# Kernel optimization log

Hardware: AMD Instinct MI355X
Metric: run time of the kernel (lower is better)

The kernel has to match this reference:

```python
import jax, jax.numpy as jnp
import numpy as np

B = 4          # number of prefill sequences (uniform cu_seqlens)
S = 1024       # tokens per sequence; total_tokens = B*S
SCALE = 0.08838834764831845  # head_dim ** -0.5


def setup_inputs() -> dict:
    key = jax.random.key(0)
    k1, k2, k3 = jax.random.split(key, 3)
    N, H, Hk, D = B * S, 16, 4, 128
    q = jax.random.normal(k1, (N, H, D), dtype=jnp.float32)
    k = jax.random.normal(k2, (N, Hk, D), dtype=jnp.float32)
    v = jax.random.normal(k3, (N, Hk, D), dtype=jnp.float32)
    k_cache = jnp.zeros((N, Hk * D), dtype=jnp.float32)
    v_cache = jnp.zeros((N, Hk * D), dtype=jnp.float32)
    slot_mapping = jnp.arange(N, dtype=jnp.int32)
    return {"q": q, "k": k, "v": v, "k_cache": k_cache,
            "v_cache": v_cache, "slot_mapping": slot_mapping}


def _store_kvcache(k, v, k_cache, v_cache, slot_mapping):
    # scatter token KV into flat paged cache; slot == -1 means skip
    N = k.shape[0]
    valid = slot_mapping >= 0
    slot = jnp.where(valid, slot_mapping, 0)
    k_flat = k.reshape(N, -1)
    v_flat = v.reshape(N, -1)
    kc = k_cache.at[slot].set(jnp.where(valid[:, None], k_flat, k_cache[slot]))
    vc = v_cache.at[slot].set(jnp.where(valid[:, None], v_flat, v_cache[slot]))
    return kc, vc


def _varlen_causal_attn(q, k, v):
    # q: [N, H, D], k/v: [N, Hk, D] with N = B*S uniform sequences (GQA)
    N, H, D = q.shape
    Hk = k.shape[1]
    G = H // Hk
    qb = q.reshape(B, S, Hk, G, D)
    kb = k.reshape(B, S, Hk, D)
    vb = v.reshape(B, S, Hk, D)
    # scores: [B, Hk, G, Sq, Sk]
    scores = jnp.einsum("bqhgd,bkhd->bhgqk", qb, kb) * jnp.float32(SCALE)
    causal = jnp.tril(jnp.ones((S, S), dtype=bool))  # [Sq, Sk]
    scores = jnp.where(causal, scores, jnp.float32(-1e30))
    p = jax.nn.softmax(scores, axis=-1)
    o = jnp.einsum("bhgqk,bkhd->bqhgd", p, vb)
    return o.reshape(N, H, D)


def reference(q, k, v, k_cache, v_cache, slot_mapping):
    kc, vc = _store_kvcache(k, v, k_cache, v_cache, slot_mapping)
    o = _varlen_causal_attn(q, k, v)
    return o, kc, vc
```

## Files before the change

kernel.cpp:

```cpp
#include <hip/hip_runtime.h>

typedef short bf16x8 __attribute__((ext_vector_type(8)));
typedef short bf16x4 __attribute__((ext_vector_type(4)));
typedef float f32x4 __attribute__((ext_vector_type(4)));
typedef float f32x16 __attribute__((ext_vector_type(16)));

#define NB 4
#define SS 1024
#define NH 16
#define NHK 4
#define DD 128
#define NT 16
#define QSCALE 0.08838834764831845f
#define LOG2E 1.4426950408889634f

__device__ __forceinline__ float exp2v(float x) { return __builtin_amdgcn_exp2f(x); }

__device__ __forceinline__ short f2bf(float f) {
  unsigned u = __builtin_bit_cast(unsigned, f);
  u += 0x7fffu + ((u >> 16) & 1u);
  return (short)(u >> 16);
}
__device__ __forceinline__ unsigned pk2(float lo, float hi) {
  return ((unsigned)(unsigned short)f2bf(hi) << 16) | (unsigned)(unsigned short)f2bf(lo);
}

typedef __attribute__((address_space(1))) const unsigned gu32;
typedef __attribute__((address_space(3))) unsigned lu32;
__device__ __forceinline__ void gload16(const void* g, void* l) {
  __builtin_amdgcn_global_load_lds((gu32*)g, (lu32*)l, 16, 0, 0);
}

#define DRAIN_DMA()                                    \
  do {                                                 \
    asm volatile("s_waitcnt vmcnt(0)" ::: "memory");   \
    __builtin_amdgcn_sched_barrier(0);                 \
  } while (0)

__global__ __launch_bounds__(256) void scatter_kv_kernel(
    const float* __restrict__ k, const float* __restrict__ v,
    const int* __restrict__ slot, float* __restrict__ ko, float* __restrict__ vo) {
  int gid = blockIdx.x * blockDim.x + threadIdx.x;
  int tok = gid >> 7;
  int j = gid & 127;
  int s = slot[tok];
  if (s < 0) return;
  ((float4*)(ko + (size_t)s * 512))[j] = ((const float4*)(k + (size_t)tok * 512))[j];
  ((float4*)(vo + (size_t)s * 512))[j] = ((const float4*)(v + (size_t)tok * 512))[j];
}

__global__ __launch_bounds__(256) void prep_kernel(
    const float* __restrict__ k, const float* __restrict__ v,
    const int* __restrict__ slot,
    short* __restrict__ kimg, short* __restrict__ vimg,
    float* __restrict__ ko, float* __restrict__ vo) {
  __shared__ float lvf[64 * 129];
  const int blk = blockIdx.x;
  const int t = blk & 15;
  const int hk = (blk >> 4) & 3;
  const int b = blk >> 6;
  const long tb = (long)b * SS + t * 64;
  const int tid = threadIdx.x;
  short* ki = kimg + (size_t)blk * 8192;
  short* vi = vimg + (size_t)blk * 8192;

#pragma unroll
  for (int p = 0; p < 4; ++p) {
    int c = p * 256 + tid;
    int byte0 = c * 16;
    int row = byte0 >> 8;
    int d0 = (byte0 & 255) >> 1;
    const float* src = k + ((tb + row) * NHK + hk) * DD + d0;
    float4 x = *(const float4*)src;
    float4 y = *(const float4*)(src + 4);
    uint4 pk = {pk2(x.x, x.y), pk2(x.z, x.w), pk2(y.x, y.y), pk2(y.z, y.w)};
    *(uint4*)((char*)ki + (byte0 ^ ((row & 15) << 4))) = pk;
    const float* vs = v + ((tb + row) * NHK + hk) * DD + d0;
    float4 vx = *(const float4*)vs;
    float4 vy = *(const float4*)(vs + 4);
    int sl = slot[tb + row];
    if (sl >= 0) {
      float* kd = ko + (size_t)sl * 512 + hk * 128 + d0;
      *(float4*)kd = x; *(float4*)(kd + 4) = y;
      float* vd = vo + (size_t)sl * 512 + hk * 128 + d0;
      *(float4*)vd = vx; *(float4*)(vd + 4) = vy;
    }
    float* dst = &lvf[row * 129 + d0];
    dst[0] = vx.x; dst[1] = vx.y; dst[2] = vx.z; dst[3] = vx.w;
    dst[4] = vy.x; dst[5] = vy.y; dst[6] = vy.z; dst[7] = vy.w;
  }
  __syncthreads();
#pragma unroll
  for (int p = 0; p < 4; ++p) {
    int c16 = p * 256 + tid;
    int d = c16 >> 3;
    int kv0 = (c16 & 7) << 3;
    float f[8];
#pragma unroll
    for (int j = 0; j < 8; ++j) f[j] = lvf[(kv0 + j) * 129 + d];
    uint4 pk = {pk2(f[0], f[1]), pk2(f[2], f[3]), pk2(f[4], f[5]), pk2(f[6], f[7])};
    int dest = (d << 7) + ((kv0 << 1) ^ ((d & 7) << 4));
    *(uint4*)((char*)vi + dest) = pk;
  }
}

__global__ __launch_bounds__(256, 2) void attn_kernel(
    const float* __restrict__ q, const short* __restrict__ kimg,
    const short* __restrict__ vimg, float* __restrict__ o) {
  __shared__ __align__(16) short lk[2][64 * 128];
  __shared__ __align__(16) short lv[2][64 * 128];

  const int tid = threadIdx.x;
  const int l = tid & 63;
  const int w = tid >> 6;
  const int hi = l >> 5;
  const int lq = l & 31;

  const int bid = blockIdx.x;
  const int x = bid & 7;
  const int s_ = bid >> 3;
  const int half = s_ >> 5;
  const int i = s_ & 31;
  const int g16 = x + (half << 3);
  const int hk = g16 & 3;
  const int b = g16 >> 2;
  const int h = hk * 4 + (i >> 3);
  const int jj0 = i & 7;
  const int jj = half ? jj0 : 7 - jj0;

  const int qbase = jj << 7;
  const int tlast = 2 * jj + 1;

  const int q_seq = qbase + (w << 5) + lq;
  const long qtok = (long)b * SS + q_seq;

  bf16x8 qf[8];
  {
    const float sc = QSCALE * LOG2E;
    const float* qrow = q + (qtok * NH + h) * DD;
#pragma unroll
    for (int ks = 0; ks < 8; ++ks) {
      int d0 = ks * 16 + hi * 8;
      float4 a = *(const float4*)(qrow + d0);
      float4 bb = *(const float4*)(qrow + d0 + 4);
      bf16x8 tt;
      tt[0] = f2bf(a.x * sc); tt[1] = f2bf(a.y * sc);
      tt[2] = f2bf(a.z * sc); tt[3] = f2bf(a.w * sc);
      tt[4] = f2bf(bb.x * sc); tt[5] = f2bf(bb.y * sc);
      tt[6] = f2bf(bb.z * sc); tt[7] = f2bf(bb.w * sc);
      qf[ks] = tt;
    }
  }

  f32x16 zeroes;
#pragma unroll
  for (int r = 0; r < 16; ++r) zeroes[r] = 0.f;
  f32x16 oacc[4];
#pragma unroll
  for (int d = 0; d < 4; ++d) oacc[d] = zeroes;
  float lsum = 0.f;

  const char* kbase = (const char*)(kimg + ((size_t)g16 * NT) * 8192);
  const char* vbase = (const char*)(vimg + ((size_t)g16 * NT) * 8192);

#define STAGE(buf, tt)                                                \
  {                                                                   \
    const char* ks_ = kbase + (size_t)(tt) * 16384;                   \
    const char* vs_ = vbase + (size_t)(tt) * 16384;                   \
    _Pragma("unroll") for (int p4 = 0; p4 < 4; ++p4) {                \
      int off = p4 * 4096 + tid * 16;                                 \
      gload16(ks_ + off, (char*)lk + (buf) * 16384 + off);            \
      gload16(vs_ + off, (char*)lv + (buf) * 16384 + off);            \
    }                                                                 \
  }

  STAGE(0, 0);
  DRAIN_DMA();
  __syncthreads();

  for (int t = 0; t <= tlast; ++t) {
    const int cur = t & 1;
    if (t < tlast) STAGE(cur ^ 1, t + 1);

    const char* lkc = (const char*)lk[cur];
    const char* lvc = (const char*)lv[cur];

    f32x16 s0 = zeroes, s1 = zeroes;
    {
      const int rb0 = lq << 8;
      const int rb1 = (32 + lq) << 8;
      const int sw = (lq & 15) << 4;
#pragma unroll
      for (int ks = 0; ks < 8; ++ks) {
        int off = ((ks << 5) + (hi << 4)) ^ sw;
        bf16x8 kf0 = *(const bf16x8*)(lkc + rb0 + off);
        bf16x8 kf1 = *(const bf16x8*)(lkc + rb1 + off);
        s0 = __builtin_amdgcn_mfma_f32_32x32x16_bf16(kf0, qf[ks], s0, 0, 0, 0);
        s1 = __builtin_amdgcn_mfma_f32_32x32x16_bf16(kf1, qf[ks], s1, 0, 0, 0);
      }
    }

    if ((t << 6) + 63 > qbase + (w << 5)) {
#pragma unroll
      for (int r = 0; r < 16; ++r) {
        int kvr = (t << 6) + (r & 3) + ((r >> 2) << 3) + (hi << 2);
        if (kvr > q_seq) s0[r] = -1e30f;
        if (kvr + 32 > q_seq) s1[r] = -1e30f;
      }
    }

    {
      float acc = 0.f;
#pragma unroll
      for (int r = 0; r < 16; ++r) {
        float p0 = exp2v(s0[r]); s0[r] = p0;
        float p1 = exp2v(s1[r]); s1[r] = p1;
        acc += p0 + p1;
      }
      lsum += acc;
    }

    bf16x8 pa[4];
#pragma unroll
    for (int sub = 0; sub < 2; ++sub) {
#pragma unroll
      for (int m = 0; m < 2; ++m) {
        f32x16 P = sub ? s1 : s0;
        unsigned A, B, C, D;
        asm("v_cvt_pk_bf16_f32 %0, %1, %2" : "=v"(A) : "v"(P[8 * m + 0]), "v"(P[8 * m + 1]));
        asm("v_cvt_pk_bf16_f32 %0, %1, %2" : "=v"(B) : "v"(P[8 * m + 2]), "v"(P[8 * m + 3]));
        asm("v_cvt_pk_bf16_f32 %0, %1, %2" : "=v"(C) : "v"(P[8 * m + 4]), "v"(P[8 * m + 5]));
        asm("v_cvt_pk_bf16_f32 %0, %1, %2" : "=v"(D) : "v"(P[8 * m + 6]), "v"(P[8 * m + 7]));
        asm("v_permlane32_swap_b32 %0, %1" : "+v"(A), "+v"(C));
        asm("v_permlane32_swap_b32 %0, %1" : "+v"(B), "+v"(D));
        union { uint4 u; bf16x8 v8; } pu;
        pu.u = uint4{A, B, C, D};
        pa[sub * 2 + m] = pu.v8;
      }
    }

#pragma unroll
    for (int ds = 0; ds < 4; ++ds) {
      const int rb = ((ds << 5) + lq) << 7;
      const int sw = (lq & 7) << 4;
#pragma unroll
      for (int m = 0; m < 4; ++m) {
        bf16x8 vf = *(const bf16x8*)(lvc + rb + (((m << 5) + (hi << 4)) ^ sw));
        oacc[ds] = __builtin_amdgcn_mfma_f32_32x32x16_bf16(pa[m], vf, oacc[ds], 0, 0, 0);
      }
    }

    DRAIN_DMA();
    __syncthreads();
  }
#undef STAGE

  lsum += __shfl_xor(lsum, 32);
#pragma unroll
  for (int r = 0; r < 16; ++r) {
    int qloc = (r & 3) + ((r >> 2) << 3) + (hi << 2);
    float inv = 1.f / __shfl(lsum, qloc);
    long tok = (long)b * SS + qbase + (w << 5) + qloc;
    float* dst = o + (tok * NH + h) * DD + lq;
    dst[0]  = oacc[0][r] * inv;
    dst[32] = oacc[1][r] * inv;
    dst[64] = oacc[2][r] * inv;
    dst[96] = oacc[3][r] * inv;
  }
}

__global__ __launch_bounds__(256) void attn_fallback(
    const float* __restrict__ q, const float* __restrict__ k,
    const float* __restrict__ v, float* __restrict__ o) {
  __shared__ short lk[64 * 128];
  __shared__ short lvt[128 * 64];
  const int tid = threadIdx.x;
  const int l = tid & 63;
  const int w = tid >> 6;
  const int lg = l >> 4;
  const int lr = l & 15;
  const int bid = blockIdx.x;
  const int qt = bid & 15;
  const int h = (bid >> 4) & 15;
  const int b = bid >> 8;
  const int hk = h >> 2;
  const int q_seq = qt * 64 + w * 16 + lr;
  const long qtok = (long)b * SS + q_seq;
  bf16x8 qf[4];
  {
    const float* qrow = q + (qtok * NH + h) * DD;
#pragma unroll
    for (int c = 0; c < 4; ++c) {
      int d0 = c * 32 + lg * 8;
      float4 a = *(const float4*)(qrow + d0);
      float4 bb = *(const float4*)(qrow + d0 + 4);
      bf16x8 t;
      t[0] = f2bf(a.x * QSCALE); t[1] = f2bf(a.y * QSCALE);
      t[2] = f2bf(a.z * QSCALE); t[3] = f2bf(a.w * QSCALE);
      t[4] = f2bf(bb.x * QSCALE); t[5] = f2bf(bb.y * QSCALE);
      t[6] = f2bf(bb.z * QSCALE); t[7] = f2bf(bb.w * QSCALE);
      qf[c] = t;
    }
  }
  f32x4 oacc[8];
#pragma unroll
  for (int i = 0; i < 8; ++i) oacc[i] = f32x4{0.f, 0.f, 0.f, 0.f};
  float m_run = -1e30f, l_run = 0.f;
  const int ntiles = qt + 1;
  for (int t = 0; t < ntiles; ++t) {
    const long tb = (long)b * SS + t * 64;
#pragma unroll
    for (int it = 0; it < 8; ++it) {
      int task = it * 256 + tid;
      int row = task >> 5;
      int dq = (task & 31) << 2;
      float4 xx = *(const float4*)(k + ((tb + row) * NHK + hk) * DD + dq);
      int byte = (row << 8) + (dq << 1);
      byte ^= (row & 7) << 4;
      *(uint2*)((char*)lk + byte) = make_uint2(pk2(xx.x, xx.y), pk2(xx.z, xx.w));
    }
    {
      int a = tid >> 3;
      int e = tid & 7;
      const float* v0r = v + ((tb + 2 * a) * NHK + hk) * DD;
      const float* v1r = v0r + NHK * DD;
#pragma unroll
      for (int i = 0; i < 4; ++i) {
        int d0 = e * 4 + i * 32;
        float4 x0 = *(const float4*)(v0r + d0);
        float4 x1 = *(const float4*)(v1r + d0);
        unsigned pw[4] = {pk2(x0.x, x1.x), pk2(x0.y, x1.y), pk2(x0.z, x1.z), pk2(x0.w, x1.w)};
#pragma unroll
        for (int j = 0; j < 4; ++j) {
          int row = d0 + j;
          int byte = (row << 7) + (a << 2);
          byte ^= (row & 7) << 4;
          *(unsigned*)((char*)lvt + byte) = pw[j];
        }
      }
    }
    __syncthreads();
    f32x4 s[4];
#pragma unroll
    for (int kt = 0; kt < 4; ++kt) {
      f32x4 acc = f32x4{0.f, 0.f, 0.f, 0.f};
      int row = kt * 16 + lr;
#pragma unroll
      for (int c = 0; c < 4; ++c) {
        int byte = (row << 8) + (c << 6) + (lg << 4);
        byte ^= (row & 7) << 4;
        bf16x8 kf = *(const bf16x8*)((const char*)lk + byte);
        acc = __builtin_amdgcn_mfma_f32_16x16x32_bf16(kf, qf[c], acc, 0, 0, 0);
      }
      s[kt] = acc;
    }
    if (t == qt) {
#pragma unroll
      for (int kt = 0; kt < 4; ++kt)
#pragma unroll
        for (int r = 0; r < 4; ++r) {
          int kvg = t * 64 + kt * 16 + lg * 4 + r;
          if (kvg > q_seq) s[kt][r] = -1e30f;
        }
    }
    float mx = -1e30f;
#pragma unroll
    for (int kt = 0; kt < 4; ++kt)
#pragma unroll
      for (int r = 0; r < 4; ++r) mx = fmaxf(mx, s[kt][r]);
    mx = fmaxf(mx, __shfl_xor(mx, 16));
    mx = fmaxf(mx, __shfl_xor(mx, 32));
    float mnew = fmaxf(m_run, mx);
    float resc = expf(m_run - mnew);
    float rsum = 0.f;
#pragma unroll
    for (int kt = 0; kt < 4; ++kt)
#pragma unroll
      for (int r = 0; r < 4; ++r) {
        float pp = expf(s[kt][r] - mnew);
        s[kt][r] = pp;
        rsum += pp;
      }
    rsum += __shfl_xor(rsum, 16);
    rsum += __shfl_xor(rsum, 32);
    l_run = l_run * resc + rsum;
    m_run = mnew;
#pragma unroll
    for (int r = 0; r < 4; ++r) {
      float fr = __shfl(resc, (lg << 2) + r);
#pragma unroll
      for (int dt = 0; dt < 8; ++dt) oacc[dt][r] *= fr;
    }
#pragma unroll
    for (int c = 0; c < 2; ++c) {
      bf16x8 pa;
#pragma unroll
      for (int r = 0; r < 4; ++r) {
        pa[r] = f2bf(s[2 * c][r]);
        pa[r + 4] = f2bf(s[2 * c + 1][r]);
      }
#pragma unroll
      for (int dt = 0; dt < 8; ++dt) {
        int d = dt * 16 + lr;
        int rowbase = d << 7;
        int sw = (d & 7) << 4;
        int b0 = rowbase + (((c << 6) + (lg << 3)) ^ sw);
        int b1 = rowbase + (((c << 6) + 32 + (lg << 3)) ^ sw);
        bf16x4 lo = *(const bf16x4*)((const char*)lvt + b0);
        bf16x4 hi2 = *(const bf16x4*)((const char*)lvt + b1);
        bf16x8 vf = __builtin_shufflevector(lo, hi2, 0, 1, 2, 3, 4, 5, 6, 7);
        oacc[dt] = __builtin_amdgcn_mfma_f32_16x16x32_bf16(pa, vf, oacc[dt], 0, 0, 0);
      }
    }
    __syncthreads();
  }
#pragma unroll
  for (int r = 0; r < 4; ++r) {
    float inv = 1.f / __shfl(l_run, (lg << 2) + r);
    long tok = (long)b * SS + qt * 64 + w * 16 + lg * 4 + r;
    float* dst = o + (tok * NH + h) * DD + lr;
#pragma unroll
    for (int dt = 0; dt < 8; ++dt) dst[dt * 16] = oacc[dt][r] * inv;
  }
}

extern "C" void kernel_launch(void* const* d_in, const int* in_sizes, int n_in,
                              void* d_out, int out_size, void* d_ws, size_t ws_size,
                              hipStream_t stream) {
  const float* q = (const float*)d_in[0];
  const float* k = (const float*)d_in[1];
  const float* v = (const float*)d_in[2];
  const int* slot = (const int*)d_in[5];

  float* out = (float*)d_out;
  float* o_out = out;
  float* k_out = out + (size_t)NB * SS * NH * DD;
  float* v_out = k_out + (size_t)NB * SS * NHK * DD;

  const size_t img_elems = (size_t)NB * NHK * NT * 8192;
  const size_t ws_need = img_elems * 2 * sizeof(short);

  if (ws_size >= ws_need) {
    short* kimg = (short*)d_ws;
    short* vimg = kimg + img_elems;
    prep_kernel<<<NB * NHK * NT, 256, 0, stream>>>(k, v, slot, kimg, vimg, k_out, v_out);
    attn_kernel<<<NB * NH * 8, 256, 0, stream>>>(q, kimg, vimg, o_out);
  } else {
    attn_fallback<<<NB * NH * (SS / 64), 256, 0, stream>>>(q, k, v, o_out);
    scatter_kv_kernel<<<(NB * SS * 128) / 256, 256, 0, stream>>>(k, v, slot, k_out, v_out);
  }
}
```

Measured before the change: 48.06 us.

## Split each KV tile across two wave groups and reduce partial outputs in LDS

The attention block grows from 256 to 512 threads. The two halves of each 64-row KV tile go to two groups of four waves, and each group computes scores and partial PV for its 32 KV rows. At the end, the upper group writes its unnormalised output accumulators and row sums to shared memory, and the lower group adds them before normalising and storing. The aim is more waves in flight and a shorter dependent MFMA chain per wave, at the cost of a cross-wave reduction, an extra barrier and repeated Q loading per group. The 4-blocks-per-CU launch bound may also tighten register limits.

```diff
diff --git a/kernel.cpp b/kernel.cpp
--- a/kernel.cpp
+++ b/kernel.cpp
@@ -104,17 +104,19 @@
   }
 }
 
-__global__ __launch_bounds__(256, 2) void attn_kernel(
+__global__ __launch_bounds__(512, 4) void attn_kernel(
     const float* __restrict__ q, const short* __restrict__ kimg,
     const short* __restrict__ vimg, float* __restrict__ o) {
-  __shared__ __align__(16) short lk[2][64 * 128];
-  __shared__ __align__(16) short lv[2][64 * 128];
+  __shared__ __align__(16) short smem[4][64 * 128];
+  __shared__ float lsums[8][64];
 
   const int tid = threadIdx.x;
   const int l = tid & 63;
   const int w = tid >> 6;
   const int hi = l >> 5;
   const int lq = l & 31;
+  const int H = w >> 2;
+  const int ws = w & 3;
 
   const int bid = blockIdx.x;
   const int x = bid & 7;
@@ -131,7 +133,7 @@
   const int qbase = jj << 7;
   const int tlast = 2 * jj + 1;
 
-  const int q_seq = qbase + (w << 5) + lq;
+  const int q_seq = qbase + (ws << 5) + lq;
   const long qtok = (long)b * SS + q_seq;
 
   bf16x8 qf[8];
@@ -167,10 +169,10 @@
   {                                                                   \
     const char* ks_ = kbase + (size_t)(tt) * 16384;                   \
     const char* vs_ = vbase + (size_t)(tt) * 16384;                   \
-    _Pragma("unroll") for (int p4 = 0; p4 < 4; ++p4) {                \
-      int off = p4 * 4096 + tid * 16;                                 \
-      gload16(ks_ + off, (char*)lk + (buf) * 16384 + off);            \
-      gload16(vs_ + off, (char*)lv + (buf) * 16384 + off);            \
+    _Pragma("unroll") for (int p4 = 0; p4 < 2; ++p4) {                \
+      int off = p4 * 8192 + tid * 16;                                 \
+      gload16(ks_ + off, (char*)smem[buf] + off);                     \
+      gload16(vs_ + off, (char*)smem[2 + (buf)] + off);               \
     }                                                                 \
   }
 
@@ -182,30 +184,25 @@
     const int cur = t & 1;
     if (t < tlast) STAGE(cur ^ 1, t + 1);
 
-    const char* lkc = (const char*)lk[cur];
-    const char* lvc = (const char*)lv[cur];
-
-    f32x16 s0 = zeroes, s1 = zeroes;
+    const char* lkc = (const char*)smem[cur];
+    const char* lvc = (const char*)smem[2 + cur];
+
+    f32x16 s = zeroes;
     {
-      const int rb0 = lq << 8;
-      const int rb1 = (32 + lq) << 8;
+      const int rb = ((H << 5) + lq) << 8;
       const int sw = (lq & 15) << 4;
 #pragma unroll
       for (int ks = 0; ks < 8; ++ks) {
-        int off = ((ks << 5) + (hi << 4)) ^ sw;
-        bf16x8 kf0 = *(const bf16x8*)(lkc + rb0 + off);
-        bf16x8 kf1 = *(const bf16x8*)(lkc + rb1 + off);
-        s0 = __builtin_amdgcn_mfma_f32_32x32x16_bf16(kf0, qf[ks], s0, 0, 0, 0);
-        s1 = __builtin_amdgcn_mfma_f32_32x32x16_bf16(kf1, qf[ks], s1, 0, 0, 0);
-      }
-    }
-
-    if ((t << 6) + 63 > qbase + (w << 5)) {
+        bf16x8 kf = *(const bf16x8*)(lkc + rb + (((ks << 5) + (hi << 4)) ^ sw));
+        s = __builtin_amdgcn_mfma_f32_32x32x16_bf16(kf, qf[ks], s, 0, 0, 0);
+      }
+    }
+
+    if ((t << 6) + (H << 5) + 31 > qbase + (ws << 5)) {
 #pragma unroll
       for (int r = 0; r < 16; ++r) {
-        int kvr = (t << 6) + (r & 3) + ((r >> 2) << 3) + (hi << 2);
-        if (kvr > q_seq) s0[r] = -1e30f;
-        if (kvr + 32 > q_seq) s1[r] = -1e30f;
+        int kvr = (t << 6) + (H << 5) + (r & 3) + ((r >> 2) << 3) + (hi << 2);
+        if (kvr > q_seq) s[r] = -1e30f;
       }
     }
 
@@ -213,39 +210,36 @@
       float acc = 0.f;
 #pragma unroll
       for (int r = 0; r < 16; ++r) {
-        float p0 = exp2v(s0[r]); s0[r] = p0;
-        float p1 = exp2v(s1[r]); s1[r] = p1;
-        acc += p0 + p1;
+        float pp = exp2v(s[r]);
+        s[r] = pp;
+        acc += pp;
       }
       lsum += acc;
     }
 
-    bf16x8 pa[4];
-#pragma unroll
-    for (int sub = 0; sub < 2; ++sub) {
+    bf16x8 pa[2];
+#pragma unroll
+    for (int m = 0; m < 2; ++m) {
+      unsigned A, B, C, D;
+      asm("v_cvt_pk_bf16_f32 %0, %1, %2" : "=v"(A) : "v"(s[8 * m + 0]), "v"(s[8 * m + 1]));
+      asm("v_cvt_pk_bf16_f32 %0, %1, %2" : "=v"(B) : "v"(s[8 * m + 2]), "v"(s[8 * m + 3]));
+      asm("v_cvt_pk_bf16_f32 %0, %1, %2" : "=v"(C) : "v"(s[8 * m + 4]), "v"(s[8 * m + 5]));
+      asm("v_cvt_pk_bf16_f32 %0, %1, %2" : "=v"(D) : "v"(s[8 * m + 6]), "v"(s[8 * m + 7]));
+      asm("v_permlane32_swap_b32 %0, %1" : "+v"(A), "+v"(C));
+      asm("v_permlane32_swap_b32 %0, %1" : "+v"(B), "+v"(D));
+      union { uint4 u; bf16x8 v8; } pu;
+      pu.u = uint4{A, B, C, D};
+      pa[m] = pu.v8;
+    }
+
+#pragma unroll
+    for (int ds = 0; ds < 4; ++ds) {
+      const int rbv = ((ds << 5) + lq) << 7;
+      const int swv = (lq & 7) << 4;
 #pragma unroll
       for (int m = 0; m < 2; ++m) {
-        f32x16 P = sub ? s1 : s0;
-        unsigned A, B, C, D;
-        asm("v_cvt_pk_bf16_f32 %0, %1, %2" : "=v"(A) : "v"(P[8 * m + 0]), "v"(P[8 * m + 1]));
-        asm("v_cvt_pk_bf16_f32 %0, %1, %2" : "=v"(B) : "v"(P[8 * m + 2]), "v"(P[8 * m + 3]));
-        asm("v_cvt_pk_bf16_f32 %0, %1, %2" : "=v"(C) : "v"(P[8 * m + 4]), "v"(P[8 * m + 5]));
-        asm("v_cvt_pk_bf16_f32 %0, %1, %2" : "=v"(D) : "v"(P[8 * m + 6]), "v"(P[8 * m + 7]));
-        asm("v_permlane32_swap_b32 %0, %1" : "+v"(A), "+v"(C));
-        asm("v_permlane32_swap_b32 %0, %1" : "+v"(B), "+v"(D));
-        union { uint4 u; bf16x8 v8; } pu;
-        pu.u = uint4{A, B, C, D};
-        pa[sub * 2 + m] = pu.v8;
-      }
-    }
-
-#pragma unroll
-    for (int ds = 0; ds < 4; ++ds) {
-      const int rb = ((ds << 5) + lq) << 7;
-      const int sw = (lq & 7) << 4;
-#pragma unroll
-      for (int m = 0; m < 4; ++m) {
-        bf16x8 vf = *(const bf16x8*)(lvc + rb + (((m << 5) + (hi << 4)) ^ sw));
+        int mm = (H << 1) + m;
+        bf16x8 vf = *(const bf16x8*)(lvc + rbv + ((((mm) << 5) + (hi << 4)) ^ swv));
         oacc[ds] = __builtin_amdgcn_mfma_f32_32x32x16_bf16(pa[m], vf, oacc[ds], 0, 0, 0);
       }
     }
@@ -255,17 +249,45 @@
   }
 #undef STAGE
 
-  lsum += __shfl_xor(lsum, 32);
-#pragma unroll
-  for (int r = 0; r < 16; ++r) {
-    int qloc = (r & 3) + ((r >> 2) << 3) + (hi << 2);
-    float inv = 1.f / __shfl(lsum, qloc);
-    long tok = (long)b * SS + qbase + (w << 5) + qloc;
-    float* dst = o + (tok * NH + h) * DD + lq;
-    dst[0]  = oacc[0][r] * inv;
-    dst[32] = oacc[1][r] * inv;
-    dst[64] = oacc[2][r] * inv;
-    dst[96] = oacc[3][r] * inv;
+  {
+    float* xch = (float*)smem;
+    lsums[w][l] = lsum;
+    if (w >= 4) {
+#pragma unroll
+      for (int ds = 0; ds < 4; ++ds)
+#pragma unroll
+        for (int g = 0; g < 4; ++g) {
+          float4 vv = {oacc[ds][4 * g], oacc[ds][4 * g + 1],
+                       oacc[ds][4 * g + 2], oacc[ds][4 * g + 3]};
+          *(float4*)&xch[(((w - 4) * 16 + ds * 4 + g) << 8) + (l << 2)] = vv;
+        }
+    }
+    __syncthreads();
+    if (w < 4) {
+      lsum += lsums[w + 4][l];
+#pragma unroll
+      for (int ds = 0; ds < 4; ++ds)
+#pragma unroll
+        for (int g = 0; g < 4; ++g) {
+          float4 vv = *(const float4*)&xch[((w * 16 + ds * 4 + g) << 8) + (l << 2)];
+          oacc[ds][4 * g]     += vv.x;
+          oacc[ds][4 * g + 1] += vv.y;
+          oacc[ds][4 * g + 2] += vv.z;
+          oacc[ds][4 * g + 3] += vv.w;
+        }
+      lsum += __shfl_xor(lsum, 32);
+#pragma unroll
+      for (int r = 0; r < 16; ++r) {
+        int qloc = (r & 3) + ((r >> 2) << 3) + (hi << 2);
+        float inv = 1.f / __shfl(lsum, qloc);
+        long tok = (long)b * SS + qbase + (ws << 5) + qloc;
+        float* dst = o + (tok * NH + h) * DD + lq;
+        dst[0]  = oacc[0][r] * inv;
+        dst[32] = oacc[1][r] * inv;
+        dst[64] = oacc[2][r] * inv;
+        dst[96] = oacc[3][r] * inv;
+      }
+    }
   }
 }
 
@@ -444,7 +466,7 @@
     short* kimg = (short*)d_ws;
     short* vimg = kimg + img_elems;
     prep_kernel<<<NB * NHK * NT, 256, 0, stream>>>(k, v, slot, kimg, vimg, k_out, v_out);
-    attn_kernel<<<NB * NH * 8, 256, 0, stream>>>(q, kimg, vimg, o_out);
+    attn_kernel<<<NB * NH * 8, 512, 0, stream>>>(q, kimg, vimg, o_out);
   } else {
     attn_fallback<<<NB * NH * (SS / 64), 256, 0, stream>>>(q, k, v, o_out);
     scatter_kv_kernel<<<(NB * SS * 128) / 256, 256, 0, stream>>>(k, v, slot, k_out, v_out);
```

Result: slower. 59.63 us (+24.1%).

## Use 512-thread blocks covering 256 queries with per-warp causal skip

Applied to the files above, without the earlier changes.

Each block now has 8 warps covering 256 query rows instead of 128. The grid shrinks to 256 blocks, one per CU, and K/V tile staging is spread over twice as many threads. Warps whose query rows lie entirely before the current KV tile skip the compute but still join the barriers. A dead shared-memory pad forces one block per CU. The lopsided causal balancing of the old mapping is gone, so blocks with larger jj2 do up to four times more tiles, which risks load imbalance.

```diff
diff --git a/kernel.cpp b/kernel.cpp
--- a/kernel.cpp
+++ b/kernel.cpp
@@ -104,11 +104,13 @@
   }
 }
 
-__global__ __launch_bounds__(256, 2) void attn_kernel(
+__global__ __launch_bounds__(512, 1) void attn_kernel(
     const float* __restrict__ q, const short* __restrict__ kimg,
     const short* __restrict__ vimg, float* __restrict__ o) {
   __shared__ __align__(16) short lk[2][64 * 128];
   __shared__ __align__(16) short lv[2][64 * 128];
+  __shared__ float deadpad[5120];
+  if (blockIdx.x == 0xFFFFFFFFu) deadpad[threadIdx.x] = 0.f;
 
   const int tid = threadIdx.x;
   const int l = tid & 63;
@@ -118,21 +120,36 @@
 
   const int bid = blockIdx.x;
   const int x = bid & 7;
-  const int s_ = bid >> 3;
-  const int half = s_ >> 5;
-  const int i = s_ & 31;
-  const int g16 = x + (half << 3);
+  const int r_ = bid >> 3;
+  const int g16 = x + ((r_ >> 4) << 3);
+  const int rr = r_ & 15;
+  const int hsub = rr >> 2;
+  const int jj2 = rr & 3;
   const int hk = g16 & 3;
   const int b = g16 >> 2;
-  const int h = hk * 4 + (i >> 3);
-  const int jj0 = i & 7;
-  const int jj = half ? jj0 : 7 - jj0;
-
-  const int qbase = jj << 7;
-  const int tlast = 2 * jj + 1;
+  const int h = hk * 4 + hsub;
+
+  const int qbase = jj2 << 8;
+  const int tlast = 4 * jj2 + 3;
 
   const int q_seq = qbase + (w << 5) + lq;
   const long qtok = (long)b * SS + q_seq;
+
+  const char* kbase = (const char*)(kimg + ((size_t)g16 * NT) * 8192);
+  const char* vbase = (const char*)(vimg + ((size_t)g16 * NT) * 8192);
+
+#define STAGE(buf, tt)                                                \
+  {                                                                   \
+    const char* ks_ = kbase + (size_t)(tt) * 16384;                   \
+    const char* vs_ = vbase + (size_t)(tt) * 16384;                   \
+    _Pragma("unroll") for (int p4 = 0; p4 < 2; ++p4) {                \
+      int off = p4 * 8192 + tid * 16;                                 \
+      gload16(ks_ + off, (char*)lk + (buf) * 16384 + off);            \
+      gload16(vs_ + off, (char*)lv + (buf) * 16384 + off);            \
+    }                                                                 \
+  }
+
+  STAGE(0, 0);
 
   bf16x8 qf[8];
   {
@@ -160,21 +177,6 @@
   for (int d = 0; d < 4; ++d) oacc[d] = zeroes;
   float lsum = 0.f;
 
-  const char* kbase = (const char*)(kimg + ((size_t)g16 * NT) * 8192);
-  const char* vbase = (const char*)(vimg + ((size_t)g16 * NT) * 8192);
-
-#define STAGE(buf, tt)                                                \
-  {                                                                   \
-    const char* ks_ = kbase + (size_t)(tt) * 16384;                   \
-    const char* vs_ = vbase + (size_t)(tt) * 16384;                   \
-    _Pragma("unroll") for (int p4 = 0; p4 < 4; ++p4) {                \
-      int off = p4 * 4096 + tid * 16;                                 \
-      gload16(ks_ + off, (char*)lk + (buf) * 16384 + off);            \
-      gload16(vs_ + off, (char*)lv + (buf) * 16384 + off);            \
-    }                                                                 \
-  }
-
-  STAGE(0, 0);
   DRAIN_DMA();
   __syncthreads();
 
@@ -182,71 +184,74 @@
     const int cur = t & 1;
     if (t < tlast) STAGE(cur ^ 1, t + 1);
 
-    const char* lkc = (const char*)lk[cur];
-    const char* lvc = (const char*)lv[cur];
-
-    f32x16 s0 = zeroes, s1 = zeroes;
-    {
-      const int rb0 = lq << 8;
-      const int rb1 = (32 + lq) << 8;
-      const int sw = (lq & 15) << 4;
-#pragma unroll
-      for (int ks = 0; ks < 8; ++ks) {
-        int off = ((ks << 5) + (hi << 4)) ^ sw;
-        bf16x8 kf0 = *(const bf16x8*)(lkc + rb0 + off);
-        bf16x8 kf1 = *(const bf16x8*)(lkc + rb1 + off);
-        s0 = __builtin_amdgcn_mfma_f32_32x32x16_bf16(kf0, qf[ks], s0, 0, 0, 0);
-        s1 = __builtin_amdgcn_mfma_f32_32x32x16_bf16(kf1, qf[ks], s1, 0, 0, 0);
-      }
-    }
-
-    if ((t << 6) + 63 > qbase + (w << 5)) {
-#pragma unroll
-      for (int r = 0; r < 16; ++r) {
-        int kvr = (t << 6) + (r & 3) + ((r >> 2) << 3) + (hi << 2);
-        if (kvr > q_seq) s0[r] = -1e30f;
-        if (kvr + 32 > q_seq) s1[r] = -1e30f;
-      }
-    }
-
-    {
-      float acc = 0.f;
-#pragma unroll
-      for (int r = 0; r < 16; ++r) {
-        float p0 = exp2v(s0[r]); s0[r] = p0;
-        float p1 = exp2v(s1[r]); s1[r] = p1;
-        acc += p0 + p1;
-      }
-      lsum += acc;
-    }
-
-    bf16x8 pa[4];
-#pragma unroll
-    for (int sub = 0; sub < 2; ++sub) {
-#pragma unroll
-      for (int m = 0; m < 2; ++m) {
-        f32x16 P = sub ? s1 : s0;
-        unsigned A, B, C, D;
-        asm("v_cvt_pk_bf16_f32 %0, %1, %2" : "=v"(A) : "v"(P[8 * m + 0]), "v"(P[8 * m + 1]));
-        asm("v_cvt_pk_bf16_f32 %0, %1, %2" : "=v"(B) : "v"(P[8 * m + 2]), "v"(P[8 * m + 3]));
-        asm("v_cvt_pk_bf16_f32 %0, %1, %2" : "=v"(C) : "v"(P[8 * m + 4]), "v"(P[8 * m + 5]));
-        asm("v_cvt_pk_bf16_f32 %0, %1, %2" : "=v"(D) : "v"(P[8 * m + 6]), "v"(P[8 * m + 7]));
-        asm("v_permlane32_swap_b32 %0, %1" : "+v"(A), "+v"(C));
-        asm("v_permlane32_swap_b32 %0, %1" : "+v"(B), "+v"(D));
-        union { uint4 u; bf16x8 v8; } pu;
-        pu.u = uint4{A, B, C, D};
-        pa[sub * 2 + m] = pu.v8;
-      }
-    }
-
-#pragma unroll
-    for (int ds = 0; ds < 4; ++ds) {
-      const int rb = ((ds << 5) + lq) << 7;
-      const int sw = (lq & 7) << 4;
-#pragma unroll
-      for (int m = 0; m < 4; ++m) {
-        bf16x8 vf = *(const bf16x8*)(lvc + rb + (((m << 5) + (hi << 4)) ^ sw));
-        oacc[ds] = __builtin_amdgcn_mfma_f32_32x32x16_bf16(pa[m], vf, oacc[ds], 0, 0, 0);
+    const bool active = (t << 6) <= qbase + (w << 5) + 31;
+    if (active) {
+      const char* lkc = (const char*)lk[cur];
+      const char* lvc = (const char*)lv[cur];
+
+      f32x16 s0 = zeroes, s1 = zeroes;
+      {
+        const int rb0 = lq << 8;
+        const int rb1 = (32 + lq) << 8;
+        const int sw = (lq & 15) << 4;
+#pragma unroll
+        for (int ks = 0; ks < 8; ++ks) {
+          int off = ((ks << 5) + (hi << 4)) ^ sw;
+          bf16x8 kf0 = *(const bf16x8*)(lkc + rb0 + off);
+          bf16x8 kf1 = *(const bf16x8*)(lkc + rb1 + off);
+          s0 = __builtin_amdgcn_mfma_f32_32x32x16_bf16(kf0, qf[ks], s0, 0, 0, 0);
+          s1 = __builtin_amdgcn_mfma_f32_32x32x16_bf16(kf1, qf[ks], s1, 0, 0, 0);
+        }
+      }
+
+      if ((t << 6) + 63 > qbase + (w << 5)) {
+#pragma unroll
+        for (int r = 0; r < 16; ++r) {
+          int kvr = (t << 6) + (r & 3) + ((r >> 2) << 3) + (hi << 2);
+          if (kvr > q_seq) s0[r] = -1e30f;
+          if (kvr + 32 > q_seq) s1[r] = -1e30f;
+        }
+      }
+
+      {
+        float acc = 0.f;
+#pragma unroll
+        for (int r = 0; r < 16; ++r) {
+          float p0 = exp2v(s0[r]); s0[r] = p0;
+          float p1 = exp2v(s1[r]); s1[r] = p1;
+          acc += p0 + p1;
+        }
+        lsum += acc;
+      }
+
+      bf16x8 pa[4];
+#pragma unroll
+      for (int sub = 0; sub < 2; ++sub) {
+#pragma unroll
+        for (int m = 0; m < 2; ++m) {
+          f32x16 P = sub ? s1 : s0;
+          unsigned A, B, C, D;
+          asm("v_cvt_pk_bf16_f32 %0, %1, %2" : "=v"(A) : "v"(P[8 * m + 0]), "v"(P[8 * m + 1]));
+          asm("v_cvt_pk_bf16_f32 %0, %1, %2" : "=v"(B) : "v"(P[8 * m + 2]), "v"(P[8 * m + 3]));
+          asm("v_cvt_pk_bf16_f32 %0, %1, %2" : "=v"(C) : "v"(P[8 * m + 4]), "v"(P[8 * m + 5]));
+          asm("v_cvt_pk_bf16_f32 %0, %1, %2" : "=v"(D) : "v"(P[8 * m + 6]), "v"(P[8 * m + 7]));
+          asm("v_permlane32_swap_b32 %0, %1" : "+v"(A), "+v"(C));
+          asm("v_permlane32_swap_b32 %0, %1" : "+v"(B), "+v"(D));
+          union { uint4 u; bf16x8 v8; } pu;
+          pu.u = uint4{A, B, C, D};
+          pa[sub * 2 + m] = pu.v8;
+        }
+      }
+
+#pragma unroll
+      for (int ds = 0; ds < 4; ++ds) {
+        const int rbv = ((ds << 5) + lq) << 7;
+        const int swv = (lq & 7) << 4;
+#pragma unroll
+        for (int m = 0; m < 4; ++m) {
+          bf16x8 vf = *(const bf16x8*)(lvc + rbv + ((((m) << 5) + (hi << 4)) ^ swv));
+          oacc[ds] = __builtin_amdgcn_mfma_f32_32x32x16_bf16(pa[m], vf, oacc[ds], 0, 0, 0);
+        }
       }
     }
 
@@ -444,7 +449,7 @@
     short* kimg = (short*)d_ws;
     short* vimg = kimg + img_elems;
     prep_kernel<<<NB * NHK * NT, 256, 0, stream>>>(k, v, slot, kimg, vimg, k_out, v_out);
-    attn_kernel<<<NB * NH * 8, 256, 0, stream>>>(q, kimg, vimg, o_out);
+    attn_kernel<<<256, 512, 0, stream>>>(q, kimg, vimg, o_out);
   } else {
     attn_fallback<<<NB * NH * (SS / 64), 256, 0, stream>>>(q, k, v, o_out);
     scatter_kv_kernel<<<(NB * SS * 128) / 256, 256, 0, stream>>>(k, v, slot, k_out, v_out);
```

Result: slower. 55.00 us (+14.4%).
